# Performance work log

Hardware: AMD Instinct MI355X
Metric: run time of the kernel (lower is better)

The kernel has to match this reference:

```python
import jax, jax.numpy as jnp
import numpy as np

# Complex-YOLO / YOLOv2 anchors (anchor_step = 2)
ANCHORS = np.array([1.08, 1.19, 3.42, 4.41, 6.63, 11.38, 9.42, 5.11, 16.62, 10.52], np.float32).reshape(5, 2)
NA = 5          # num_anchors
NC = 8          # num_classes
COORD_SCALE = 1.0
NOOBJECT_SCALE = 1.0
OBJECT_SCALE = 10.0
CLASS_SCALE = 1.0
SIL_THRESH = 0.6

B, H, W, T = 32, 32, 64, 50


def setup_inputs() -> dict:
    key = jax.random.key(0)
    k1, k2 = jax.random.split(key)
    output = jax.random.normal(k1, (B, NA * (7 + NC), H, W), dtype=jnp.float32)
    # target layout: (cls, x, y, w, l, im, re), normalized coords in (0,1); col 1 != 0 => valid box
    target = jax.random.uniform(k2, (B, T, 7), dtype=jnp.float32, minval=0.01, maxval=1.0)
    return {"output": output, "target": target}


def _iou_cxcywh(b1, b2):
    # b1, b2: (..., 4) as (cx, cy, w, h); axis-aligned IoU, matching bbox_ious(x1y1x2y2=False)
    mx = jnp.minimum(b1[..., 0] - b1[..., 2] / 2, b2[..., 0] - b2[..., 2] / 2)
    Mx = jnp.maximum(b1[..., 0] + b1[..., 2] / 2, b2[..., 0] + b2[..., 2] / 2)
    my = jnp.minimum(b1[..., 1] - b1[..., 3] / 2, b2[..., 1] - b2[..., 3] / 2)
    My = jnp.maximum(b1[..., 1] + b1[..., 3] / 2, b2[..., 1] + b2[..., 3] / 2)
    cw = b1[..., 2] + b2[..., 2] - (Mx - mx)
    ch = b1[..., 3] + b2[..., 3] - (My - my)
    inter = jnp.where((cw > 0) & (ch > 0), cw * ch, 0.0)
    union = b1[..., 2] * b1[..., 3] + b2[..., 2] * b2[..., 3] - inter
    return inter / union


def _region_loss(output, target):
    nB, _, nH, nW = output.shape
    anc = jnp.asarray(ANCHORS)  # [NA, 2]
    out = output.reshape(nB, NA, 7 + NC, nH, nW)
    x = jax.nn.sigmoid(out[:, :, 0])
    y = jax.nn.sigmoid(out[:, :, 1])
    w = out[:, :, 2]
    l = out[:, :, 3]
    im = out[:, :, 4]
    re = out[:, :, 5]
    conf = jax.nn.sigmoid(out[:, :, 6])
    cls_logits = jnp.moveaxis(out[:, :, 7:], 2, -1)  # [B, A, H, W, C]

    # ---- decoded pred boxes (detached, like .data in torch) ----
    sg = jax.lax.stop_gradient
    grid_x = jnp.arange(nW, dtype=jnp.float32)
    grid_y = jnp.arange(nH, dtype=jnp.float32)
    pbx = sg(x) + grid_x[None, None, None, :]
    pby = sg(y) + grid_y[None, None, :, None]
    pbw = jnp.exp(sg(w)) * anc[None, :, 0, None, None]
    pbl = jnp.exp(sg(l)) * anc[None, :, 1, None, None]
    pred = jnp.stack([pbx, pby, pbw, pbl], axis=-1).reshape(nB, NA * nH * nW, 4)  # [B, N, 4]

    # ---- build_targets (fully vectorized) ----
    tgt = sg(target)
    nT = tgt.shape[1]
    valid = jnp.cumprod((tgt[..., 1] != 0).astype(jnp.int32), axis=1).astype(bool)  # break-on-zero semantics
    gx = tgt[..., 1] * nW
    gy = tgt[..., 2] * nH
    gw = tgt[..., 3] * nW
    gl = tgt[..., 4] * nH
    gi = jnp.clip(gx.astype(jnp.int32), 0, nW - 1)
    gj = jnp.clip(gy.astype(jnp.int32), 0, nH - 1)
    gt = jnp.stack([gx, gy, gw, gl], axis=-1)  # [B, T, 4]

    # IoU of every pred box against every GT -> silence mask
    ious = _iou_cxcywh(gt[:, :, None, :], pred[:, None, :, :])  # [B, T, N]
    ious = jnp.where(valid[..., None], ious, 0.0)
    max_iou = ious.max(axis=1)  # [B, N]
    conf_mask = jnp.where(max_iou > SIL_THRESH, 0.0, NOOBJECT_SCALE).reshape(nB, NA, nH, nW)

    # anchor matching: IoU of (0,0,gw,gl) vs (0,0,aw,ah) -> closed form
    inter_a = jnp.minimum(gw[..., None], anc[None, None, :, 0]) * jnp.minimum(gl[..., None], anc[None, None, :, 1])
    union_a = (gw * gl)[..., None] + (anc[:, 0] * anc[:, 1])[None, None, :] - inter_a
    a_iou = inter_a / union_a  # [B, T, A]
    best_n = jnp.argmax(a_iou, axis=-1)
    aw = anc[best_n, 0]
    al = anc[best_n, 1]

    # winner cell per GT; later GTs overwrite earlier ones at the same cell (torch loop order)
    b_idx = jnp.arange(nB)[:, None]
    lin = ((b_idx * NA + best_n) * nH + gj) * nW + gi  # [B, T]
    M = nB * NA * nH * nW
    t_eff = jnp.where(valid, jnp.arange(nT)[None, :], -1)
    seg = jax.ops.segment_max(t_eff.reshape(-1), lin.reshape(-1), num_segments=M)
    keep = valid & (t_eff == seg[lin])
    lin_safe = jnp.where(keep, lin, M).reshape(-1)  # route losers to dummy slot

    def scat(vals):
        return jnp.zeros(M + 1, jnp.float32).at[lin_safe].set(vals.reshape(-1))[:M].reshape(nB, NA, nH, nW)

    cm = scat(keep.astype(jnp.float32))           # coord_mask == cls_mask
    tx = scat(gx - gi)
    ty = scat(gy - gj)
    tw = scat(jnp.log(gw / aw))
    tl = scat(jnp.log(gl / al))
    tim = scat(tgt[..., 5])
    tre = scat(tgt[..., 6])
    tcls = scat(tgt[..., 0]).astype(jnp.int32)

    n_idx = best_n * (nH * nW) + gj * nW + gi
    pb = pred[b_idx, n_idx]                       # [B, T, 4] pred box at winner cell
    tconf = scat(_iou_cxcywh(gt, pb))
    conf_mask = jnp.where(cm > 0, OBJECT_SCALE, conf_mask)

    # ---- masked losses ----
    def mse(p, t):
        return jnp.sum((p * cm - t * cm) ** 2)

    loss_x = COORD_SCALE * mse(x, tx)
    loss_y = COORD_SCALE * mse(y, ty)
    loss_w = COORD_SCALE * mse(w, tw)
    loss_l = COORD_SCALE * mse(l, tl)
    loss_im = COORD_SCALE * mse(im, tim)
    loss_re = COORD_SCALE * mse(re, tre)
    loss_conf = jnp.sum((conf * conf_mask - tconf * conf_mask) ** 2)
    ce = jax.nn.logsumexp(cls_logits, axis=-1) - jnp.take_along_axis(cls_logits, tcls[..., None], axis=-1)[..., 0]
    loss_cls = CLASS_SCALE * jnp.sum(cm * ce)
    return loss_x + loss_y + loss_w + loss_l + loss_conf + loss_cls + loss_im + loss_re


def reference(output, target):
    return _region_loss(output, target)
```

## Files before the change

kernel.cpp:

```cpp
#include <hip/hip_runtime.h>
#include <math.h>

#define NB 32
#define NA 5
#define NC 8
#define NH 32
#define NW 64
#define NT 50
#define NCH (7 + NC)
#define HW (NH * NW)
#define OBJECT_SCALE 10.0f

__constant__ float c_anchors[NA * 2] = {
    1.08f, 1.19f, 3.42f, 4.41f, 6.63f, 11.38f, 9.42f, 5.11f, 16.62f, 10.52f};

__device__ __forceinline__ float fast_exp(float v) { return __expf(v); }
__device__ __forceinline__ float fast_log(float v) { return __logf(v); }
__device__ __forceinline__ float fast_sigmoid(float v) {
    return __builtin_amdgcn_rcpf(1.0f + __expf(-v));
}

__global__ void prep_kernel(const float* __restrict__ target,
                            int* __restrict__ nvalid,
                            float* __restrict__ tinfo,
                            float* __restrict__ out) {
    int b = blockIdx.x;
    int t = threadIdx.x;
    const float* tp = target + (size_t)(b * NT + t) * 7;

    float t0 = 0.f, t1 = 0.f, t2 = 0.f, t3 = 0.f, t4 = 0.f, t5 = 0.f, t6 = 0.f;
    if (t < NT) {
        t0 = tp[0]; t1 = tp[1]; t2 = tp[2]; t3 = tp[3];
        t4 = tp[4]; t5 = tp[5]; t6 = tp[6];
    }
    unsigned long long bal = __ballot(t < NT && t1 != 0.0f);
    if (t == 0) {
        int nv = __ffsll((unsigned long long)~bal) - 1;
        nvalid[b] = nv;
        if (b == 0) out[0] = 0.0f;
    }
    if (t >= NT) return;

    float gx = t1 * (float)NW;
    float gy = t2 * (float)NH;
    float gw = t3 * (float)NW;
    float gl = t4 * (float)NH;

    int best_n = 0;
    float best = -1.0f;
#pragma unroll
    for (int a = 0; a < NA; ++a) {
        float aw = c_anchors[2 * a], al = c_anchors[2 * a + 1];
        float inter = fminf(gw, aw) * fminf(gl, al);
        float uni = gw * gl + aw * al - inter;
        float iou = inter / uni;
        if (iou > best) { best = iou; best_n = a; }
    }
    float aw = c_anchors[2 * best_n], al = c_anchors[2 * best_n + 1];

    int gi = min(max((int)gx, 0), NW - 1);
    int gj = min(max((int)gy, 0), NH - 1);

    float* ti = tinfo + (size_t)(b * NT + t) * 16;
    float area = gw * gl;
    ti[0] = gx - gw * 0.5f;
    ti[1] = gx + gw * 0.5f;
    ti[2] = gy - gl * 0.5f;
    ti[3] = gy + gl * 0.5f;
    ti[4] = gw;
    ti[5] = gl;
    ti[6] = 0.6f * area;
    ti[7] = (float)((best_n << 12) | (gj << 6) | gi);
    ti[8] = gx - (float)gi;
    ti[9] = gy - (float)gj;
    ti[10] = t5;
    ti[11] = t6;
    ti[12] = t0;
    ti[13] = fast_log(gw / aw);
    ti[14] = fast_log(gl / al);
    ti[15] = area;
}

__global__ __launch_bounds__(256) void cell_kernel(const float* __restrict__ output,
                                                   const float* __restrict__ tinfo,
                                                   const int* __restrict__ nvalid,
                                                   float* __restrict__ out) {
    const int blocks_per_b = (NA * HW) / 256;
    int b = blockIdx.x / blocks_per_b;
    int m = (blockIdx.x % blocks_per_b) * 256 + threadIdx.x;
    int a = m >> 11;
    int rem = m & (HW - 1);
    int j = rem >> 6;
    int i = rem & (NW - 1);

    const float* op = output + (size_t)(b * NA + a) * NCH * HW + (j << 6) + i;
    float o0 = op[0 * HW], o1 = op[1 * HW], o2 = op[2 * HW], o3 = op[3 * HW];
    float o4 = op[4 * HW], o5 = op[5 * HW], o6 = op[6 * HW];

    float x = fast_sigmoid(o0);
    float y = fast_sigmoid(o1);
    float conf = fast_sigmoid(o6);

    float aw = c_anchors[2 * a], al = c_anchors[2 * a + 1];
    float pbx = x + (float)i;
    float pby = y + (float)j;
    float pbw = fast_exp(o2) * aw;
    float pbl = fast_exp(o3) * al;

    float plx = pbx - pbw * 0.5f;
    float phx = pbx + pbw * 0.5f;
    float ply = pby - pbl * 0.5f;
    float phy = pby + pbl * 0.5f;
    float parea = pbw * pbl;
    float mycode = (float)((a << 12) | (j << 6) | i);

    int nv = nvalid[b];
    const float* tb = tinfo + (size_t)b * NT * 16;

    float silm = -1e30f;
    int ta = -1;
    for (int t = 0; t < nv; ++t) {
        const float* ti = tb + t * 16;
        float tlx = ti[0], thx = ti[1], tly = ti[2], thy = ti[3];
        float gw = ti[4], gl = ti[5], ct = ti[6], code = ti[7];
        float mx = fminf(tlx, plx);
        float Mx = fmaxf(thx, phx);
        float my = fminf(tly, ply);
        float My = fmaxf(thy, phy);
        float cw = gw + pbw - (Mx - mx);
        float ch = gl + pbl - (My - my);
        float inter = fmaxf(cw, 0.0f) * fmaxf(ch, 0.0f);
        silm = fmaxf(silm, 1.6f * inter - ct);
        if (code == mycode) ta = t;
    }

    float loss;
    if (ta >= 0) {
        const float* ti = tb + (size_t)ta * 16;
        float tlx = ti[0], thx = ti[1], tly = ti[2], thy = ti[3];
        float gw = ti[4], gl = ti[5], tarea = ti[15];
        float mx = fminf(tlx, plx);
        float Mx = fmaxf(thx, phx);
        float my = fminf(tly, ply);
        float My = fmaxf(thy, phy);
        float cw = gw + pbw - (Mx - mx);
        float ch = gl + pbl - (My - my);
        float inter = fmaxf(cw, 0.0f) * fmaxf(ch, 0.0f);
        float tconf = inter / (tarea + parea - inter);

        float dx = x - ti[8];
        float dy = y - ti[9];
        float dw = o2 - ti[13];
        float dl = o3 - ti[14];
        float di = o4 - ti[10];
        float dr = o5 - ti[11];
        loss = dx * dx + dy * dy + dw * dw + dl * dl + di * di + dr * dr;

        float dc = OBJECT_SCALE * (conf - tconf);
        loss += dc * dc;

        float cl[NC];
#pragma unroll
        for (int c = 0; c < NC; ++c) cl[c] = op[(size_t)(7 + c) * HW];
        int tcls = min(max((int)ti[12], 0), NC - 1);
        float mxl = cl[0];
#pragma unroll
        for (int c = 1; c < NC; ++c) mxl = fmaxf(mxl, cl[c]);
        float s = 0.0f;
#pragma unroll
        for (int c = 0; c < NC; ++c) s += fast_exp(cl[c] - mxl);
        loss += (mxl + fast_log(s)) - cl[tcls];
    } else {
        bool silenced = silm > 0.6f * parea;
        loss = silenced ? 0.0f : conf * conf;
    }

    for (int off = 32; off > 0; off >>= 1)
        loss += __shfl_down(loss, off, 64);
    __shared__ float s_part[4];
    int wave = threadIdx.x >> 6;
    int lane = threadIdx.x & 63;
    if (lane == 0) s_part[wave] = loss;
    __syncthreads();
    if (threadIdx.x == 0)
        atomicAdd(out, s_part[0] + s_part[1] + s_part[2] + s_part[3]);
}

extern "C" void kernel_launch(void* const* d_in, const int* in_sizes, int n_in,
                              void* d_out, int out_size, void* d_ws, size_t ws_size,
                              hipStream_t stream) {
    const float* output = (const float*)d_in[0];
    const float* target = (const float*)d_in[1];
    float* out = (float*)d_out;
    int* nvalid = (int*)d_ws;
    float* tinfo = (float*)((char*)d_ws + 128);

    hipLaunchKernelGGL(prep_kernel, dim3(NB), dim3(64), 0, stream,
                       target, nvalid, tinfo, out);
    hipLaunchKernelGGL(cell_kernel, dim3(NB * 40), dim3(256), 0, stream,
                       output, tinfo, nvalid, out);
}
```

Measured before the change: 92.07 us.

## Split target info into hot/cold arrays and simplify silence IoU test

Splits the per-target table into a compact 8-float array used by the per-cell scan loop and a second array read only by the matched cell. The overlap test is rewritten algebraically as min/max intersection widths, and the IoU threshold is refolded so each loop iteration needs a single fma (constant 0.375 = 0.6/1.6). The loads of channels 4 and 5 move into the matched branch. This cuts the loop's uniform loads and ALU work per target, at the cost of slightly different float rounding in the threshold comparison.

```diff
diff --git a/kernel.cpp b/kernel.cpp
--- a/kernel.cpp
+++ b/kernel.cpp
@@ -22,7 +22,8 @@
 
 __global__ void prep_kernel(const float* __restrict__ target,
                             int* __restrict__ nvalid,
-                            float* __restrict__ tinfo,
+                            float* __restrict__ tA,
+                            float* __restrict__ tB,
                             float* __restrict__ out) {
     int b = blockIdx.x;
     int t = threadIdx.x;
@@ -61,28 +62,31 @@
     int gi = min(max((int)gx, 0), NW - 1);
     int gj = min(max((int)gy, 0), NH - 1);
 
-    float* ti = tinfo + (size_t)(b * NT + t) * 16;
     float area = gw * gl;
-    ti[0] = gx - gw * 0.5f;
-    ti[1] = gx + gw * 0.5f;
-    ti[2] = gy - gl * 0.5f;
-    ti[3] = gy + gl * 0.5f;
-    ti[4] = gw;
-    ti[5] = gl;
-    ti[6] = 0.6f * area;
-    ti[7] = (float)((best_n << 12) | (gj << 6) | gi);
-    ti[8] = gx - (float)gi;
-    ti[9] = gy - (float)gj;
-    ti[10] = t5;
-    ti[11] = t6;
-    ti[12] = t0;
-    ti[13] = fast_log(gw / aw);
-    ti[14] = fast_log(gl / al);
-    ti[15] = area;
+    float* a8 = tA + (size_t)(b * NT + t) * 8;
+    a8[0] = gx - gw * 0.5f;
+    a8[1] = gx + gw * 0.5f;
+    a8[2] = gy - gl * 0.5f;
+    a8[3] = gy + gl * 0.5f;
+    a8[4] = 0.375f * area;
+    a8[5] = (float)((best_n << 12) | (gj << 6) | gi);
+    a8[6] = 0.f;
+    a8[7] = 0.f;
+
+    float* b8 = tB + (size_t)(b * NT + t) * 8;
+    b8[0] = gx - (float)gi;
+    b8[1] = gy - (float)gj;
+    b8[2] = t5;
+    b8[3] = t6;
+    b8[4] = t0;
+    b8[5] = fast_log(gw / aw);
+    b8[6] = fast_log(gl / al);
+    b8[7] = area;
 }
 
 __global__ __launch_bounds__(256) void cell_kernel(const float* __restrict__ output,
-                                                   const float* __restrict__ tinfo,
+                                                   const float* __restrict__ tA,
+                                                   const float* __restrict__ tB,
                                                    const int* __restrict__ nvalid,
                                                    float* __restrict__ out) {
     const int blocks_per_b = (NA * HW) / 256;
@@ -95,7 +99,7 @@
 
     const float* op = output + (size_t)(b * NA + a) * NCH * HW + (j << 6) + i;
     float o0 = op[0 * HW], o1 = op[1 * HW], o2 = op[2 * HW], o3 = op[3 * HW];
-    float o4 = op[4 * HW], o5 = op[5 * HW], o6 = op[6 * HW];
+    float o6 = op[6 * HW];
 
     float x = fast_sigmoid(o0);
     float y = fast_sigmoid(o1);
@@ -115,45 +119,41 @@
     float mycode = (float)((a << 12) | (j << 6) | i);
 
     int nv = nvalid[b];
-    const float* tb = tinfo + (size_t)b * NT * 16;
+    const float* tb8 = tA + (size_t)b * NT * 8;
 
     float silm = -1e30f;
     int ta = -1;
+#pragma unroll 2
     for (int t = 0; t < nv; ++t) {
-        const float* ti = tb + t * 16;
+        const float* ti = tb8 + t * 8;
         float tlx = ti[0], thx = ti[1], tly = ti[2], thy = ti[3];
-        float gw = ti[4], gl = ti[5], ct = ti[6], code = ti[7];
-        float mx = fminf(tlx, plx);
-        float Mx = fmaxf(thx, phx);
-        float my = fminf(tly, ply);
-        float My = fmaxf(thy, phy);
-        float cw = gw + pbw - (Mx - mx);
-        float ch = gl + pbl - (My - my);
-        float inter = fmaxf(cw, 0.0f) * fmaxf(ch, 0.0f);
-        silm = fmaxf(silm, 1.6f * inter - ct);
+        float ct2 = ti[4], code = ti[5];
+        float cw = fminf(thx, phx) - fmaxf(tlx, plx);
+        float ch = fminf(thy, phy) - fmaxf(tly, ply);
+        float cwc = fmaxf(cw, 0.0f);
+        float chc = fmaxf(ch, 0.0f);
+        silm = fmaxf(silm, __builtin_fmaf(cwc, chc, -ct2));
         if (code == mycode) ta = t;
     }
 
     float loss;
     if (ta >= 0) {
-        const float* ti = tb + (size_t)ta * 16;
-        float tlx = ti[0], thx = ti[1], tly = ti[2], thy = ti[3];
-        float gw = ti[4], gl = ti[5], tarea = ti[15];
-        float mx = fminf(tlx, plx);
-        float Mx = fmaxf(thx, phx);
-        float my = fminf(tly, ply);
-        float My = fmaxf(thy, phy);
-        float cw = gw + pbw - (Mx - mx);
-        float ch = gl + pbl - (My - my);
+        const float* ai = tb8 + (size_t)ta * 8;
+        const float* bi = tB + ((size_t)b * NT + ta) * 8;
+        float tlx = ai[0], thx = ai[1], tly = ai[2], thy = ai[3];
+        float tarea = bi[7];
+        float cw = fminf(thx, phx) - fmaxf(tlx, plx);
+        float ch = fminf(thy, phy) - fmaxf(tly, ply);
         float inter = fmaxf(cw, 0.0f) * fmaxf(ch, 0.0f);
         float tconf = inter / (tarea + parea - inter);
 
-        float dx = x - ti[8];
-        float dy = y - ti[9];
-        float dw = o2 - ti[13];
-        float dl = o3 - ti[14];
-        float di = o4 - ti[10];
-        float dr = o5 - ti[11];
+        float o4 = op[4 * HW], o5 = op[5 * HW];
+        float dx = x - bi[0];
+        float dy = y - bi[1];
+        float dw = o2 - bi[5];
+        float dl = o3 - bi[6];
+        float di = o4 - bi[2];
+        float dr = o5 - bi[3];
         loss = dx * dx + dy * dy + dw * dw + dl * dl + di * di + dr * dr;
 
         float dc = OBJECT_SCALE * (conf - tconf);
@@ -162,7 +162,7 @@
         float cl[NC];
 #pragma unroll
         for (int c = 0; c < NC; ++c) cl[c] = op[(size_t)(7 + c) * HW];
-        int tcls = min(max((int)ti[12], 0), NC - 1);
+        int tcls = min(max((int)bi[4], 0), NC - 1);
         float mxl = cl[0];
 #pragma unroll
         for (int c = 1; c < NC; ++c) mxl = fmaxf(mxl, cl[c]);
@@ -171,7 +171,7 @@
         for (int c = 0; c < NC; ++c) s += fast_exp(cl[c] - mxl);
         loss += (mxl + fast_log(s)) - cl[tcls];
     } else {
-        bool silenced = silm > 0.6f * parea;
+        bool silenced = silm > 0.375f * parea;
         loss = silenced ? 0.0f : conf * conf;
     }
 
@@ -193,10 +193,11 @@
     const float* target = (const float*)d_in[1];
     float* out = (float*)d_out;
     int* nvalid = (int*)d_ws;
-    float* tinfo = (float*)((char*)d_ws + 128);
+    float* tA = (float*)((char*)d_ws + 128);
+    float* tB = tA + (size_t)NB * NT * 8;
 
     hipLaunchKernelGGL(prep_kernel, dim3(NB), dim3(64), 0, stream,
-                       target, nvalid, tinfo, out);
+                       target, nvalid, tA, tB, out);
     hipLaunchKernelGGL(cell_kernel, dim3(NB * 40), dim3(256), 0, stream,
-                       output, tinfo, nvalid, out);
-}
+                       output, tA, tB, nvalid, out);
+}
```

After: 89.05 us. 3.3% less time.
